# Performance work log

Measured on AMD Instinct MI355X. Metric: run time of the kernel, lower is better.

Reference implementation:

```python
import jax, jax.numpy as jnp
import numpy as np

D_MODEL = 2048
NUM_Q_HEADS = 32
NUM_KV_HEADS = 8
HEAD_DIM = D_MODEL // NUM_Q_HEADS  # 64
NUM_GROUPS = NUM_Q_HEADS // NUM_KV_HEADS  # 4


def setup_inputs() -> dict:
    key = jax.random.key(0)
    ks = jax.random.split(key, 9)
    s = 1.0 / np.sqrt(D_MODEL)
    x = jax.random.normal(ks[0], (2, 2048, D_MODEL), dtype=jnp.float32)
    Wq = jax.random.uniform(ks[1], (D_MODEL, NUM_Q_HEADS * HEAD_DIM), jnp.float32, -s, s)
    bq = jax.random.uniform(ks[2], (NUM_Q_HEADS * HEAD_DIM,), jnp.float32, -s, s)
    Wk = jax.random.uniform(ks[3], (D_MODEL, NUM_KV_HEADS * HEAD_DIM), jnp.float32, -s, s)
    bk = jax.random.uniform(ks[4], (NUM_KV_HEADS * HEAD_DIM,), jnp.float32, -s, s)
    Wv = jax.random.uniform(ks[5], (D_MODEL, NUM_KV_HEADS * HEAD_DIM), jnp.float32, -s, s)
    bv = jax.random.uniform(ks[6], (NUM_KV_HEADS * HEAD_DIM,), jnp.float32, -s, s)
    Wo = jax.random.uniform(ks[7], (D_MODEL, D_MODEL), jnp.float32, -s, s)
    bo = jax.random.uniform(ks[8], (D_MODEL,), jnp.float32, -s, s)
    return {"x": x, "Wq": Wq, "bq": bq, "Wk": Wk, "bk": bk,
            "Wv": Wv, "bv": bv, "Wo": Wo, "bo": bo}


def reference(x, Wq, bq, Wk, bk, Wv, bv, Wo, bo):
    B, T, C = x.shape
    Hkv, G, Dh = NUM_KV_HEADS, NUM_GROUPS, HEAD_DIM
    # projections
    q = (x @ Wq + bq).reshape(B, T, Hkv, G, Dh)   # group G query heads per kv head
    k = (x @ Wk + bk).reshape(B, T, Hkv, Dh)
    v = (x @ Wv + bv).reshape(B, T, Hkv, Dh)
    scale = 1.0 / np.sqrt(Dh).astype(np.float32)
    # scores: [B, Hkv, G, T, T] (kv head broadcast over its G query heads)
    scores = jnp.einsum('btkgd,bskd->bkgts', q, k) * scale
    attn = jax.nn.softmax(scores, axis=-1)
    out = jnp.einsum('bkgts,bskd->btkgd', attn, v).reshape(B, T, C)
    return out @ Wo + bo
```

## Files before the change

kernel.cpp:

```cpp
#include <hip/hip_runtime.h>
#include <cstdint>
#include <cstddef>
#include <math.h>

typedef uint16_t bf16;
typedef __attribute__((ext_vector_type(8))) __bf16 bf16x8;
typedef __attribute__((ext_vector_type(4))) float f32x4;
typedef __attribute__((ext_vector_type(16))) float f32x16;

#define MFMA16(a,b,c) __builtin_amdgcn_mfma_f32_16x16x32_bf16((a),(b),(c),0,0,0)
#define MFMA32(a,b,c) __builtin_amdgcn_mfma_f32_32x32x16_bf16((a),(b),(c),0,0,0)

__device__ __forceinline__ uint16_t f2bf(float f){
  uint32_t u = __float_as_uint(f);
  return (uint16_t)((u + 0x7fffu + ((u >> 16) & 1u)) >> 16);
}
__device__ __forceinline__ uint32_t pk2(float lo, float hi){
  return (uint32_t)f2bf(lo) | ((uint32_t)f2bf(hi) << 16);
}

__device__ __forceinline__ void gload_lds16(const void* g, void* l){
  __builtin_amdgcn_global_load_lds((const __attribute__((address_space(1))) void*)g,
                                   (__attribute__((address_space(3))) void*)l, 16, 0, 0);
}

__global__ void k_convert(const float* __restrict__ in, bf16* __restrict__ out, int n){
  int i = (blockIdx.x * 256 + threadIdx.x) * 4;
  if (i >= n) return;
  float4 v = *reinterpret_cast<const float4*>(in + i);
  uint32_t lo = pk2(v.x, v.y);
  uint32_t hi = pk2(v.z, v.w);
  uint2 pkv = make_uint2(lo, hi);
  *reinterpret_cast<uint2*>(out + i) = pkv;
}

__global__ void k_transposeW(const float* __restrict__ in, bf16* __restrict__ out, int R, int C){
  __shared__ float tile[32][33];
  int c0 = blockIdx.x * 32, r0 = blockIdx.y * 32;
  int tx = threadIdx.x, ty = threadIdx.y;
  #pragma unroll
  for (int i = 0; i < 4; i++)
    tile[ty + 8*i][tx] = in[(size_t)(r0 + ty + 8*i) * C + c0 + tx];
  __syncthreads();
  #pragma unroll
  for (int i = 0; i < 4; i++)
    out[(size_t)(c0 + ty + 8*i) * R + r0 + tx] = f2bf(tile[tx][ty + 8*i]);
}

__global__ void k_transposeV(const bf16* __restrict__ v, bf16* __restrict__ vt){
  __shared__ bf16 tile[32][33];
  int c0 = blockIdx.x * 32, r0 = blockIdx.y * 32;
  int tx = threadIdx.x, ty = threadIdx.y;
  #pragma unroll
  for (int i = 0; i < 4; i++)
    tile[ty + 8*i][tx] = v[(size_t)(r0 + ty + 8*i) * 512 + c0 + tx];
  __syncthreads();
  int b = r0 >> 11; int t0 = r0 & 2047;
  #pragma unroll
  for (int i = 0; i < 4; i++)
    vt[((size_t)b * 512 + c0 + ty + 8*i) * 2048 + t0 + tx] = tile[tx][ty + 8*i];
}

__device__ __forceinline__ void gemm128_core(
    const bf16* __restrict__ Abase, const bf16* __restrict__ Btbase,
    int lda, int ldb, int K, bf16* As, bf16* Bs, f32x4 acc[4][4])
{
  const int tid = threadIdx.x;
  const int wid = tid >> 6, lane = tid & 63;
  const int wr = wid >> 1, wc = wid & 1;
  const int lr = lane & 15, lg = lane >> 4;
  const f32x4 vzero = {0.f, 0.f, 0.f, 0.f};

  #pragma unroll
  for (int m = 0; m < 4; m++)
    #pragma unroll
    for (int n = 0; n < 4; n++)
      acc[m][n] = vzero;

  int srcA[4], srcB[4], dOff[4];
  #pragma unroll
  for (int i = 0; i < 4; i++){
    int d = i*4096 + wid*1024 + lane*16;
    int row = d >> 7, sp = (d >> 4) & 7;
    int sl = sp ^ (row & 7);
    srcA[i] = row * lda + sl * 8;
    srcB[i] = row * ldb + sl * 8;
    dOff[i] = i*4096 + wid*1024;
  }

  for (int k0 = 0; k0 < K; k0 += 64){
    #pragma unroll
    for (int i = 0; i < 4; i++)
      gload_lds16(Abase + k0 + srcA[i], (char*)As + dOff[i]);
    #pragma unroll
    for (int i = 0; i < 4; i++)
      gload_lds16(Btbase + k0 + srcB[i], (char*)Bs + dOff[i]);
    __syncthreads();
    #pragma unroll
    for (int ks = 0; ks < 2; ks++){
      bf16x8 af[4], bfr[4];
      #pragma unroll
      for (int m = 0; m < 4; m++){
        int row = wr*64 + m*16 + lr;
        int sp = (ks*4 + lg) ^ (row & 7);
        af[m] = *reinterpret_cast<const bf16x8*>(As + row*64 + sp*8);
      }
      #pragma unroll
      for (int n = 0; n < 4; n++){
        int row = wc*64 + n*16 + lr;
        int sp = (ks*4 + lg) ^ (row & 7);
        bfr[n] = *reinterpret_cast<const bf16x8*>(Bs + row*64 + sp*8);
      }
      #pragma unroll
      for (int m = 0; m < 4; m++)
        #pragma unroll
        for (int n = 0; n < 4; n++)
          acc[m][n] = MFMA16(af[m], bfr[n], acc[m][n]);
    }
    __syncthreads();
  }
}

__global__ __launch_bounds__(256, 2) void k_qkv(
    const bf16* __restrict__ xb,
    const bf16* __restrict__ WqT, const bf16* __restrict__ WkT, const bf16* __restrict__ WvT,
    const float* __restrict__ bq, const float* __restrict__ bk, const float* __restrict__ bv,
    bf16* __restrict__ qo, bf16* __restrict__ ko, bf16* __restrict__ vo)
{
  __shared__ __align__(16) bf16 As[128*64];
  __shared__ __align__(16) bf16 Bs[128*64];
  int by = blockIdx.y;
  const bf16* Bt; const float* bias; bf16* outp; int ldc; float scale;
  if (by < 16){      Bt = WqT + (size_t)by*128*2048;      bias = bq + by*128;      outp = qo + by*128;      ldc = 2048; scale = 0.18033688011112042f; }
  else if (by < 20){ int y = by-16; Bt = WkT + (size_t)y*128*2048; bias = bk + y*128; outp = ko + y*128; ldc = 512;  scale = 1.f; }
  else {             int y = by-20; Bt = WvT + (size_t)y*128*2048; bias = bv + y*128; outp = vo + y*128; ldc = 512;  scale = 1.f; }
  int m0 = blockIdx.x * 128;
  f32x4 acc[4][4];
  gemm128_core(xb + (size_t)m0*2048, Bt, 2048, 2048, 2048, As, Bs, acc);
  const int tid = threadIdx.x, wid = tid >> 6, lane = tid & 63;
  const int wr = wid >> 1, wc = wid & 1, lr = lane & 15, lg = lane >> 4;
  #pragma unroll
  for (int n = 0; n < 4; n++){
    int col = wc*64 + n*16 + lr;
    float bb = bias[col];
    #pragma unroll
    for (int m = 0; m < 4; m++)
      #pragma unroll
      for (int r = 0; r < 4; r++){
        int row = m0 + wr*64 + m*16 + lg*4 + r;
        outp[(size_t)row*ldc + col] = f2bf((acc[m][n][r] + bb) * scale);
      }
  }
}

__global__ __launch_bounds__(256, 2) void k_oproj(
    const bf16* __restrict__ ab, const bf16* __restrict__ WoT,
    const float* __restrict__ bo, float* __restrict__ outp)
{
  __shared__ __align__(16) bf16 As[128*64];
  __shared__ __align__(16) bf16 Bs[128*64];
  int m0 = blockIdx.x * 128, n0 = blockIdx.y * 128;
  f32x4 acc[4][4];
  gemm128_core(ab + (size_t)m0*2048, WoT + (size_t)n0*2048, 2048, 2048, 2048, As, Bs, acc);
  const int tid = threadIdx.x, wid = tid >> 6, lane = tid & 63;
  const int wr = wid >> 1, wc = wid & 1, lr = lane & 15, lg = lane >> 4;
  #pragma unroll
  for (int n = 0; n < 4; n++){
    int col = n0 + wc*64 + n*16 + lr;
    float bb = bo[col];
    #pragma unroll
    for (int m = 0; m < 4; m++)
      #pragma unroll
      for (int r = 0; r < 4; r++){
        int row = m0 + wr*64 + m*16 + lg*4 + r;
        outp[(size_t)row*2048 + col] = acc[m][n][r] + bb;
      }
  }
}

__global__ __launch_bounds__(256, 2) void k_flash(
    const bf16* __restrict__ q, const bf16* __restrict__ kmat,
    const bf16* __restrict__ vt, bf16* __restrict__ ao)
{
  __shared__ __align__(16) bf16 Ks[2][64*64];
  __shared__ __align__(16) bf16 Vs[2][64*64];
  const int tid = threadIdx.x;
  const int wid = tid >> 6, lane = tid & 63;
  const int l31 = lane & 31, hi = lane >> 5;
  const int bh = blockIdx.y;
  const int b = bh >> 5, hq = bh & 31, kvh = hq >> 2;
  const int qt = blockIdx.x;
  const int qrow0 = b*2048 + qt*128 + wid*32;

  bf16x8 qf[4];
  {
    const bf16* qrow = q + (size_t)(qrow0 + l31)*2048 + hq*64 + hi*8;
    #pragma unroll
    for (int t = 0; t < 4; t++)
      qf[t] = *reinterpret_cast<const bf16x8*>(qrow + t*16);
  }

  f32x16 oacc[2];
  #pragma unroll
  for (int n = 0; n < 2; n++)
    #pragma unroll
    for (int r = 0; r < 16; r++) oacc[n][r] = 0.f;
  f32x4 rsv = {0.f, 0.f, 0.f, 0.f};

  const bf16* kbase = kmat + (size_t)b*2048*512 + kvh*64;
  const bf16* vbase = vt + ((size_t)b*512 + kvh*64)*2048;

  int kSrc[2], vSrc[2], dOff[2];
  #pragma unroll
  for (int i = 0; i < 2; i++){
    int db = i*4096 + wid*1024 + lane*16;
    int row = db >> 7, sp = (db >> 4) & 7;
    int sl = sp ^ (row & 7);
    kSrc[i] = row*512  + sl*8;
    vSrc[i] = row*2048 + sl*8;
    dOff[i] = i*4096 + wid*1024;
  }

  #define STAGE(buf, st_) do { \
    const bf16* kb_ = kbase + (size_t)(st_)*64*512; \
    const bf16* vb_ = vbase + (st_)*64; \
    gload_lds16(kb_ + kSrc[0], (char*)Ks[buf] + dOff[0]); \
    gload_lds16(kb_ + kSrc[1], (char*)Ks[buf] + dOff[1]); \
    gload_lds16(vb_ + vSrc[0], (char*)Vs[buf] + dOff[0]); \
    gload_lds16(vb_ + vSrc[1], (char*)Vs[buf] + dOff[1]); \
  } while(0)

  STAGE(0, 0);
  __syncthreads();

  for (int st = 0; st < 32; st++){
    int cur = st & 1;
    if (st < 31) STAGE(cur^1, st+1);

    f32x16 sc[2];
    #pragma unroll
    for (int n = 0; n < 2; n++)
      #pragma unroll
      for (int r = 0; r < 16; r++) sc[n][r] = 0.f;
    __builtin_amdgcn_s_setprio(1);
    #pragma unroll
    for (int t = 0; t < 4; t++){
      bf16x8 af[2];
      #pragma unroll
      for (int n = 0; n < 2; n++){
        int row = 32*n + l31;
        int ph = (2*t + hi) ^ (row & 7);
        af[n] = *reinterpret_cast<const bf16x8*>(Ks[cur] + row*64 + ph*8);
      }
      #pragma unroll
      for (int n = 0; n < 2; n++)
        sc[n] = MFMA32(af[n], qf[t], sc[n]);
    }
    __builtin_amdgcn_s_setprio(0);

    uint32_t pw[2][8];
    #pragma unroll
    for (int n = 0; n < 2; n++)
      #pragma unroll
      for (int j = 0; j < 8; j++){
        float plo = __builtin_amdgcn_exp2f(sc[n][2*j]);
        float phi = __builtin_amdgcn_exp2f(sc[n][2*j+1]);
        rsv[j & 3] += plo + phi;
        asm("v_cvt_pk_bf16_f32 %0, %1, %2" : "=v"(pw[n][j]) : "v"(plo), "v"(phi));
      }
    #pragma unroll
    for (int n = 0; n < 2; n++)
      #pragma unroll
      for (int h = 0; h < 2; h++){
        asm volatile("v_permlane32_swap_b32 %0, %1" : "+v"(pw[n][h*4+0]), "+v"(pw[n][h*4+2]));
        asm volatile("v_permlane32_swap_b32 %0, %1" : "+v"(pw[n][h*4+1]), "+v"(pw[n][h*4+3]));
      }

    __builtin_amdgcn_s_setprio(1);
    #pragma unroll
    for (int kk = 0; kk < 4; kk++){
      int n = kk >> 1, h = kk & 1;
      union { uint32_t w[4]; bf16x8 v; } pa;
      pa.w[0] = pw[n][h*4+0]; pa.w[1] = pw[n][h*4+1];
      pa.w[2] = pw[n][h*4+2]; pa.w[3] = pw[n][h*4+3];
      bf16x8 vf[2];
      #pragma unroll
      for (int nd = 0; nd < 2; nd++){
        int row = 32*nd + l31;
        int ph = (2*kk + hi) ^ (row & 7);
        vf[nd] = *reinterpret_cast<const bf16x8*>(Vs[cur] + row*64 + ph*8);
      }
      #pragma unroll
      for (int nd = 0; nd < 2; nd++)
        oacc[nd] = MFMA32(pa.v, vf[nd], oacc[nd]);
    }
    __builtin_amdgcn_s_setprio(0);
    __syncthreads();
  }
  #undef STAGE

  float rs = (rsv[0] + rsv[1]) + (rsv[2] + rsv[3]);
  float l = rs + __shfl_xor(rs, 32);
  float linv = 1.f / l;
  float lv[16];
  #pragma unroll
  for (int r = 0; r < 16; r++){
    int qi = (r & 3) + 8*(r >> 2) + 4*hi;
    lv[r] = __shfl(linv, qi);
  }
  #pragma unroll
  for (int nd = 0; nd < 2; nd++)
    #pragma unroll
    for (int r = 0; r < 16; r++){
      int qi = (r & 3) + 8*(r >> 2) + 4*hi;
      int row = qrow0 + qi;
      ao[(size_t)row*2048 + hq*64 + nd*32 + l31] = f2bf(oacc[nd][r] * lv[r]);
    }
}

extern "C" void kernel_launch(void* const* d_in, const int* in_sizes, int n_in,
                              void* d_out, int out_size, void* d_ws, size_t ws_size,
                              hipStream_t stream)
{
  const float* x  = (const float*)d_in[0];
  const float* Wq = (const float*)d_in[1];
  const float* bq = (const float*)d_in[2];
  const float* Wk = (const float*)d_in[3];
  const float* bk = (const float*)d_in[4];
  const float* Wv = (const float*)d_in[5];
  const float* bv = (const float*)d_in[6];
  const float* Wo = (const float*)d_in[7];
  const float* bo = (const float*)d_in[8];
  float* out = (float*)d_out;

  char* ws = (char*)d_ws;
  size_t off = 0;
  auto alloc = [&](size_t bytes){ char* p = ws + off; off += (bytes + 255) & ~(size_t)255; return p; };
  bf16* xb  = (bf16*)alloc(2*2048*2048*2);
  bf16* WqT = (bf16*)alloc(2048*2048*2);
  bf16* WkT = (bf16*)alloc(512*2048*2);
  bf16* WvT = (bf16*)alloc(512*2048*2);
  bf16* WoT = (bf16*)alloc(2048*2048*2);
  bf16* qb  = (bf16*)alloc(4096*2048*2);
  bf16* kb  = (bf16*)alloc((size_t)4096*512*2);
  bf16* vb  = (bf16*)alloc((size_t)4096*512*2);
  bf16* vtb = (bf16*)alloc((size_t)4096*512*2);
  bf16* aob = xb;

  k_convert<<<8192, 256, 0, stream>>>(x, xb, 2*2048*2048);
  k_transposeW<<<dim3(64,64), dim3(32,8), 0, stream>>>(Wq, WqT, 2048, 2048);
  k_transposeW<<<dim3(16,64), dim3(32,8), 0, stream>>>(Wk, WkT, 2048, 512);
  k_transposeW<<<dim3(16,64), dim3(32,8), 0, stream>>>(Wv, WvT, 2048, 512);
  k_transposeW<<<dim3(64,64), dim3(32,8), 0, stream>>>(Wo, WoT, 2048, 2048);
  k_qkv<<<dim3(32,24), 256, 0, stream>>>(xb, WqT, WkT, WvT, bq, bk, bv, qb, kb, vb);
  k_transposeV<<<dim3(16,128), dim3(32,8), 0, stream>>>(vb, vtb);
  k_flash<<<dim3(16,64), 256, 0, stream>>>(qb, kb, vtb, aob);
  k_oproj<<<dim3(32,16), 256, 0, stream>>>(aob, WoT, bo, out);
}
```

Before: 204.7 us.

## Enlarge flash attention tiles to 256 queries and 128-key stages with 512 threads

The flash kernel now runs 8 waves (512 threads) per block, covering 256 query rows, and stages 128 keys per pipeline step, so each K/V tile loaded into LDS is shared by twice as many queries and there are half as many block barriers. The QK^T chain starts from a zero-vector constant instead of explicitly zeroed accumulators, and the row-sum accumulation uses packed float2 adds. LDS use doubles to 64 KB per block, and the grid halves to 512 blocks, which may reduce occupancy and raise register pressure under the 512-thread, 4-wave-per-EU launch bound.

```diff
diff --git a/kernel.cpp b/kernel.cpp
--- a/kernel.cpp
+++ b/kernel.cpp
@@ -5,6 +5,7 @@
 
 typedef uint16_t bf16;
 typedef __attribute__((ext_vector_type(8))) __bf16 bf16x8;
+typedef __attribute__((ext_vector_type(2))) float f32x2;
 typedef __attribute__((ext_vector_type(4))) float f32x4;
 typedef __attribute__((ext_vector_type(16))) float f32x16;
 
@@ -178,19 +179,19 @@
   }
 }
 
-__global__ __launch_bounds__(256, 2) void k_flash(
+__global__ __launch_bounds__(512, 4) void k_flash(
     const bf16* __restrict__ q, const bf16* __restrict__ kmat,
     const bf16* __restrict__ vt, bf16* __restrict__ ao)
 {
-  __shared__ __align__(16) bf16 Ks[2][64*64];
-  __shared__ __align__(16) bf16 Vs[2][64*64];
+  __shared__ __align__(16) bf16 Ks[2][128*64];
+  __shared__ __align__(16) bf16 Vs[2][64*128];
   const int tid = threadIdx.x;
   const int wid = tid >> 6, lane = tid & 63;
   const int l31 = lane & 31, hi = lane >> 5;
   const int bh = blockIdx.y;
   const int b = bh >> 5, hq = bh & 31, kvh = hq >> 2;
   const int qt = blockIdx.x;
-  const int qrow0 = b*2048 + qt*128 + wid*32;
+  const int qrow0 = b*2048 + qt*256 + wid*32;
 
   bf16x8 qf[4];
   {
@@ -205,7 +206,10 @@
   for (int n = 0; n < 2; n++)
     #pragma unroll
     for (int r = 0; r < 16; r++) oacc[n][r] = 0.f;
-  f32x4 rsv = {0.f, 0.f, 0.f, 0.f};
+  f32x2 rp[4];
+  #pragma unroll
+  for (int j = 0; j < 4; j++){ rp[j][0] = 0.f; rp[j][1] = 0.f; }
+  const f32x16 zv = {0.f,0.f,0.f,0.f,0.f,0.f,0.f,0.f,0.f,0.f,0.f,0.f,0.f,0.f,0.f,0.f};
 
   const bf16* kbase = kmat + (size_t)b*2048*512 + kvh*64;
   const bf16* vbase = vt + ((size_t)b*512 + kvh*64)*2048;
@@ -213,17 +217,17 @@
   int kSrc[2], vSrc[2], dOff[2];
   #pragma unroll
   for (int i = 0; i < 2; i++){
-    int db = i*4096 + wid*1024 + lane*16;
-    int row = db >> 7, sp = (db >> 4) & 7;
-    int sl = sp ^ (row & 7);
-    kSrc[i] = row*512  + sl*8;
-    vSrc[i] = row*2048 + sl*8;
-    dOff[i] = i*4096 + wid*1024;
+    int db = i*8192 + tid*16;
+    int krow = db >> 7, ksp = (db >> 4) & 7,  ksl = ksp ^ (krow & 7);
+    int vrow = db >> 8, vsp = (db >> 4) & 15, vsl = vsp ^ (vrow & 7);
+    kSrc[i] = krow*512  + ksl*8;
+    vSrc[i] = vrow*2048 + vsl*8;
+    dOff[i] = i*8192 + wid*1024;
   }
 
   #define STAGE(buf, st_) do { \
-    const bf16* kb_ = kbase + (size_t)(st_)*64*512; \
-    const bf16* vb_ = vbase + (st_)*64; \
+    const bf16* kb_ = kbase + (size_t)(st_)*128*512; \
+    const bf16* vb_ = vbase + (st_)*128; \
     gload_lds16(kb_ + kSrc[0], (char*)Ks[buf] + dOff[0]); \
     gload_lds16(kb_ + kSrc[1], (char*)Ks[buf] + dOff[1]); \
     gload_lds16(vb_ + vSrc[0], (char*)Vs[buf] + dOff[0]); \
@@ -233,73 +237,86 @@
   STAGE(0, 0);
   __syncthreads();
 
-  for (int st = 0; st < 32; st++){
+  for (int st = 0; st < 16; st++){
     int cur = st & 1;
-    if (st < 31) STAGE(cur^1, st+1);
-
-    f32x16 sc[2];
-    #pragma unroll
-    for (int n = 0; n < 2; n++)
-      #pragma unroll
-      for (int r = 0; r < 16; r++) sc[n][r] = 0.f;
-    __builtin_amdgcn_s_setprio(1);
-    #pragma unroll
-    for (int t = 0; t < 4; t++){
-      bf16x8 af[2];
-      #pragma unroll
-      for (int n = 0; n < 2; n++){
-        int row = 32*n + l31;
-        int ph = (2*t + hi) ^ (row & 7);
-        af[n] = *reinterpret_cast<const bf16x8*>(Ks[cur] + row*64 + ph*8);
-      }
+    if (st < 15) STAGE(cur^1, st+1);
+
+    #pragma unroll
+    for (int c = 0; c < 2; c++){
+      f32x16 sc[2];
+      __builtin_amdgcn_s_setprio(1);
+      {
+        bf16x8 af[2];
+        #pragma unroll
+        for (int n = 0; n < 2; n++){
+          int row = 64*c + 32*n + l31;
+          int ph = hi ^ (row & 7);
+          af[n] = *reinterpret_cast<const bf16x8*>(Ks[cur] + row*64 + ph*8);
+        }
+        #pragma unroll
+        for (int n = 0; n < 2; n++)
+          sc[n] = MFMA32(af[n], qf[0], zv);
+      }
+      #pragma unroll
+      for (int t = 1; t < 4; t++){
+        bf16x8 af[2];
+        #pragma unroll
+        for (int n = 0; n < 2; n++){
+          int row = 64*c + 32*n + l31;
+          int ph = (2*t + hi) ^ (row & 7);
+          af[n] = *reinterpret_cast<const bf16x8*>(Ks[cur] + row*64 + ph*8);
+        }
+        #pragma unroll
+        for (int n = 0; n < 2; n++)
+          sc[n] = MFMA32(af[n], qf[t], sc[n]);
+      }
+      __builtin_amdgcn_s_setprio(0);
+
+      uint32_t pw[2][8];
       #pragma unroll
       for (int n = 0; n < 2; n++)
-        sc[n] = MFMA32(af[n], qf[t], sc[n]);
+        #pragma unroll
+        for (int j = 0; j < 8; j++){
+          float plo = __builtin_amdgcn_exp2f(sc[n][2*j]);
+          float phi = __builtin_amdgcn_exp2f(sc[n][2*j+1]);
+          f32x2 e; e[0] = plo; e[1] = phi;
+          rp[j & 3] += e;
+          asm("v_cvt_pk_bf16_f32 %0, %1, %2" : "=v"(pw[n][j]) : "v"(plo), "v"(phi));
+        }
+      #pragma unroll
+      for (int n = 0; n < 2; n++)
+        #pragma unroll
+        for (int h = 0; h < 2; h++){
+          asm volatile("v_permlane32_swap_b32 %0, %1" : "+v"(pw[n][h*4+0]), "+v"(pw[n][h*4+2]));
+          asm volatile("v_permlane32_swap_b32 %0, %1" : "+v"(pw[n][h*4+1]), "+v"(pw[n][h*4+3]));
+        }
+
+      __builtin_amdgcn_s_setprio(1);
+      #pragma unroll
+      for (int kk = 0; kk < 4; kk++){
+        int n = kk >> 1, h = kk & 1;
+        union { uint32_t w[4]; bf16x8 v; } pa;
+        pa.w[0] = pw[n][h*4+0]; pa.w[1] = pw[n][h*4+1];
+        pa.w[2] = pw[n][h*4+2]; pa.w[3] = pw[n][h*4+3];
+        bf16x8 vf[2];
+        #pragma unroll
+        for (int nd = 0; nd < 2; nd++){
+          int row = 32*nd + l31;
+          int ph = (8*c + 2*kk + hi) ^ (row & 7);
+          vf[nd] = *reinterpret_cast<const bf16x8*>(Vs[cur] + row*128 + ph*8);
+        }
+        #pragma unroll
+        for (int nd = 0; nd < 2; nd++)
+          oacc[nd] = MFMA32(pa.v, vf[nd], oacc[nd]);
+      }
+      __builtin_amdgcn_s_setprio(0);
     }
-    __builtin_amdgcn_s_setprio(0);
-
-    uint32_t pw[2][8];
-    #pragma unroll
-    for (int n = 0; n < 2; n++)
-      #pragma unroll
-      for (int j = 0; j < 8; j++){
-        float plo = __builtin_amdgcn_exp2f(sc[n][2*j]);
-        float phi = __builtin_amdgcn_exp2f(sc[n][2*j+1]);
-        rsv[j & 3] += plo + phi;
-        asm("v_cvt_pk_bf16_f32 %0, %1, %2" : "=v"(pw[n][j]) : "v"(plo), "v"(phi));
-      }
-    #pragma unroll
-    for (int n = 0; n < 2; n++)
-      #pragma unroll
-      for (int h = 0; h < 2; h++){
-        asm volatile("v_permlane32_swap_b32 %0, %1" : "+v"(pw[n][h*4+0]), "+v"(pw[n][h*4+2]));
-        asm volatile("v_permlane32_swap_b32 %0, %1" : "+v"(pw[n][h*4+1]), "+v"(pw[n][h*4+3]));
-      }
-
-    __builtin_amdgcn_s_setprio(1);
-    #pragma unroll
-    for (int kk = 0; kk < 4; kk++){
-      int n = kk >> 1, h = kk & 1;
-      union { uint32_t w[4]; bf16x8 v; } pa;
-      pa.w[0] = pw[n][h*4+0]; pa.w[1] = pw[n][h*4+1];
-      pa.w[2] = pw[n][h*4+2]; pa.w[3] = pw[n][h*4+3];
-      bf16x8 vf[2];
-      #pragma unroll
-      for (int nd = 0; nd < 2; nd++){
-        int row = 32*nd + l31;
-        int ph = (2*kk + hi) ^ (row & 7);
-        vf[nd] = *reinterpret_cast<const bf16x8*>(Vs[cur] + row*64 + ph*8);
-      }
-      #pragma unroll
-      for (int nd = 0; nd < 2; nd++)
-        oacc[nd] = MFMA32(pa.v, vf[nd], oacc[nd]);
-    }
-    __builtin_amdgcn_s_setprio(0);
     __syncthreads();
   }
   #undef STAGE
 
-  float rs = (rsv[0] + rsv[1]) + (rsv[2] + rsv[3]);
+  float rs = (rp[0][0] + rp[0][1]) + (rp[1][0] + rp[1][1])
+           + (rp[2][0] + rp[2][1]) + (rp[3][0] + rp[3][1]);
   float l = rs + __shfl_xor(rs, 32);
   float linv = 1.f / l;
   float lv[16];
@@ -354,6 +371,6 @@
   k_transposeW<<<dim3(64,64), dim3(32,8), 0, stream>>>(Wo, WoT, 2048, 2048);
   k_qkv<<<dim3(32,24), 256, 0, stream>>>(xb, WqT, WkT, WvT, bq, bk, bv, qb, kb, vb);
   k_transposeV<<<dim3(16,128), dim3(32,8), 0, stream>>>(vb, vtb);
-  k_flash<<<dim3(16,64), 256, 0, stream>>>(qb, kb, vtb, aob);
+  k_flash<<<dim3(8,64), 512, 0, stream>>>(qb, kb, vtb, aob);
   k_oproj<<<dim3(32,16), 256, 0, stream>>>(aob, WoT, bo, out);
 }
```

New measurement: 199.5 us. -2.5%, faster.
